# Performance work log

Measured on AMD Instinct MI355X. Metric: run time of the kernel, lower is better.

The kernel has to match this reference:

```python
import jax, jax.numpy as jnp
import numpy as np

D_MODEL = 1024
N_HEADS = 16
HEAD_DIM = D_MODEL // N_HEADS
LENGTHS = np.array([1536, 1024, 1400, 900, 1200, 1300, 1500, 1000])
OFFSETS = np.concatenate([[0], np.cumsum(LENGTHS)]).astype(np.int32)
N_TOT = int(OFFSETS[-1])
LN_EPS = 1e-5


def _pad_meta(offsets):
    # Static (numpy) gather indices: ragged concat [N,D] -> padded [B,Lmax,D]
    offsets = np.asarray(offsets)
    lengths = np.diff(offsets)
    lmax = int(lengths.max())
    tok = np.arange(lmax)[None, :]                      # [1, Lmax]
    valid = tok < lengths[:, None]                      # [B, Lmax] bool
    src = np.where(valid, offsets[:-1, None] + tok, 0)  # [B, Lmax] int
    return src, valid


def setup_inputs() -> dict:
    key = jax.random.key(0)
    ks = jax.random.split(key, 4)
    s = 1.0 / np.sqrt(D_MODEL)
    return {
        "x": jax.random.normal(ks[0], (N_TOT, D_MODEL), jnp.float32),
        "batch_offsets": jnp.asarray(OFFSETS, jnp.int32),
        "in_proj_w": jax.random.normal(ks[1], (3 * D_MODEL, D_MODEL), jnp.float32) * s,
        "in_proj_b": jnp.zeros((3 * D_MODEL,), jnp.float32),
        "out_w": jax.random.normal(ks[2], (D_MODEL, D_MODEL), jnp.float32) * s,
        "out_b": jnp.zeros((D_MODEL,), jnp.float32),
        "ln_g": jnp.ones((D_MODEL,), jnp.float32),
        "ln_b": jnp.zeros((D_MODEL,), jnp.float32),
    }


def reference(x, batch_offsets, in_proj_w, in_proj_b, out_w, out_b, ln_g, ln_b):
    src, valid = _pad_meta(np.asarray(batch_offsets))
    B, L = valid.shape
    vmask = jnp.asarray(valid)
    # deconcat_add_batch_dim: pad to [B, L, D]
    xp = x[src] * vmask[..., None]
    # pre-LayerNorm
    mu = jnp.mean(xp, axis=-1, keepdims=True)
    var = jnp.mean((xp - mu) ** 2, axis=-1, keepdims=True)
    h = (xp - mu) * jax.lax.rsqrt(var + LN_EPS) * ln_g + ln_b
    # fused qkv projection (torch MHA in_proj)
    qkv = h @ in_proj_w.T + in_proj_b                   # [B, L, 3D]
    q, k, v = jnp.split(qkv, 3, axis=-1)
    def heads(t):
        return t.reshape(B, L, N_HEADS, HEAD_DIM).transpose(0, 2, 1, 3)
    q, k, v = heads(q), heads(k), heads(v)              # [B, H, L, hd]
    scores = jnp.einsum("bhqd,bhkd->bhqk", q, k) / np.sqrt(HEAD_DIM)
    scores = jnp.where(vmask[:, None, None, :], scores, -jnp.inf)
    attn = jax.nn.softmax(scores, axis=-1)
    o = jnp.einsum("bhqk,bhkd->bhqd", attn, v)          # [B, H, L, hd]
    o = o.transpose(0, 2, 1, 3).reshape(B, L, D_MODEL)
    o = o @ out_w.T + out_b
    y = xp + o                                          # residual (dropout p=0)
    # remove_batch_dim_and_concat: unpad back to [N, D]
    return y[vmask]
```

## Files before the change

### kernel.cpp

```cpp
#include <hip/hip_runtime.h>
#include <hip/hip_bf16.h>
#include <stdint.h>

#define D_MODEL 1024
#define QKV_LD  3072
#define N_TOT   9860
#define M_PAD   9984
#define LN_EPS  1e-5f

typedef __bf16 bf16_t;
typedef __bf16 bf16x8 __attribute__((ext_vector_type(8)));
typedef float  f32x4  __attribute__((ext_vector_type(4)));
typedef float  f32x16 __attribute__((ext_vector_type(16)));
typedef uint32_t u32x4 __attribute__((ext_vector_type(4)));

__device__ inline unsigned short f2bf(float f) {
  __bf16 h = (__bf16)f;
  return __builtin_bit_cast(unsigned short, h);
}
__device__ inline int imin(int a, int b) { return a < b ? a : b; }

__device__ inline void plswap(uint32_t& a, uint32_t& b) {
  asm("v_permlane32_swap_b32 %0, %1" : "+v"(a), "+v"(b));
}

__device__ inline void gload_lds16(const bf16_t* g, void* l) {
  __builtin_amdgcn_global_load_lds(
      (const __attribute__((address_space(1))) unsigned int*)g,
      (__attribute__((address_space(3))) unsigned int*)l, 16, 0, 0);
}

__global__ __launch_bounds__(256) void cvt_weights(const float* __restrict__ w_in,
                                                   const float* __restrict__ w_out,
                                                   bf16_t* __restrict__ win,
                                                   bf16_t* __restrict__ wout) {
  const int n_in = QKV_LD * D_MODEL / 4;
  int i = blockIdx.x * 256 + threadIdx.x;
  const float* src;
  ushort4* dst;
  int j;
  if (i < n_in) { src = w_in; dst = (ushort4*)win; j = i; }
  else          { src = w_out; dst = (ushort4*)wout; j = i - n_in; }
  float4 v = ((const float4*)src)[j];
  dst[j] = make_ushort4(f2bf(v.x), f2bf(v.y), f2bf(v.z), f2bf(v.w));
}

__global__ __launch_bounds__(256) void ln_kernel(const float* __restrict__ x,
                                                 const float* __restrict__ g,
                                                 const float* __restrict__ b,
                                                 bf16_t* __restrict__ hout) {
  int row = blockIdx.x;
  int t = threadIdx.x;
  if (row >= N_TOT) {
    ((ushort4*)(hout + (size_t)row * D_MODEL))[t] = make_ushort4(0, 0, 0, 0);
    return;
  }
  float4 v = ((const float4*)(x + (size_t)row * D_MODEL))[t];
  float s  = v.x + v.y + v.z + v.w;
  float sq = v.x * v.x + v.y * v.y + v.z * v.z + v.w * v.w;
  #pragma unroll
  for (int off = 1; off < 64; off <<= 1) {
    s  += __shfl_xor(s, off);
    sq += __shfl_xor(sq, off);
  }
  __shared__ float ss[4], ssq[4];
  int wid = t >> 6;
  if ((t & 63) == 0) { ss[wid] = s; ssq[wid] = sq; }
  __syncthreads();
  s  = ss[0] + ss[1] + ss[2] + ss[3];
  sq = ssq[0] + ssq[1] + ssq[2] + ssq[3];
  float mu  = s * (1.0f / 1024.0f);
  float var = sq * (1.0f / 1024.0f) - mu * mu;
  float rs  = rsqrtf(var + LN_EPS);
  float4 gv = ((const float4*)g)[t];
  float4 bv = ((const float4*)b)[t];
  ushort4 o;
  o.x = f2bf((v.x - mu) * rs * gv.x + bv.x);
  o.y = f2bf((v.y - mu) * rs * gv.y + bv.y);
  o.z = f2bf((v.z - mu) * rs * gv.z + bv.z);
  o.w = f2bf((v.w - mu) * rs * gv.w + bv.w);
  ((ushort4*)(hout + (size_t)row * D_MODEL))[t] = o;
}

template<int NCOLS>
__global__ __launch_bounds__(512) void gemm256(const bf16_t* __restrict__ A,
                                               const bf16_t* __restrict__ B,
                                               const float* __restrict__ bias,
                                               bf16_t* __restrict__ Cbf) {
  constexpr int K = 1024, NKT = K / 64;
  constexpr int GX = M_PAD / 256;
  constexpr int NWG = GX * (NCOLS / 256);
  int bid = blockIdx.x;
  {
    constexpr int q = NWG / 8, r = NWG % 8;
    int x = bid & 7, o = bid >> 3;
    bid = (x < r ? x * (q + 1) : r * (q + 1) + (x - r) * q) + o;
  }
  const int tileM = bid % GX;
  const int tileN = bid / GX;
  const int t = threadIdx.x;
  const int lane = t & 63, wid = t >> 6;
  const int wr = wid >> 2, wc = wid & 3;

  __shared__ bf16_t As[2][256 * 64];
  __shared__ bf16_t Bs[2][256 * 64];

  f32x4 acc[8][4];
  #pragma unroll
  for (int m = 0; m < 8; ++m)
    #pragma unroll
    for (int n = 0; n < 4; ++n)
      acc[m][n] = f32x4{0.f, 0.f, 0.f, 0.f};

  const int rowA0 = tileM * 256, rowB0 = tileN * 256;
  const int lrow = lane >> 3;
  const int lch  = lane & 7;

  auto stage = [&](int buf, int kt) {
    const int k0 = kt * 64;
    #pragma unroll
    for (int i = 0; i < 4; ++i) {
      const int r  = wid * 32 + i * 8 + lrow;
      const int sc = lch ^ (r & 7);
      gload_lds16(A + (size_t)(rowA0 + r) * K + k0 + sc * 8,
                  (char*)&As[buf][(wid * 32 + i * 8) * 64]);
      gload_lds16(B + (size_t)(rowB0 + r) * K + k0 + sc * 8,
                  (char*)&Bs[buf][(wid * 32 + i * 8) * 64]);
    }
  };

  stage(0, 0);

  for (int kt = 0; kt < NKT; ++kt) {
    const int cur = kt & 1;
    if (kt + 1 < NKT) {
      stage(cur ^ 1, kt + 1);
      asm volatile("s_waitcnt vmcnt(8)" ::: "memory");
    } else {
      asm volatile("s_waitcnt vmcnt(0)" ::: "memory");
    }
    __builtin_amdgcn_s_barrier();
    __builtin_amdgcn_sched_barrier(0);

    const char* Ab = (const char*)&As[cur][0];
    const char* Bb = (const char*)&Bs[cur][0];

    bf16x8 bfr[4][2];
    #pragma unroll
    for (int n = 0; n < 4; ++n)
      #pragma unroll
      for (int ks = 0; ks < 2; ++ks) {
        int r = wc * 64 + n * 16 + (lane & 15);
        int c = ks * 4 + (lane >> 4);
        bfr[n][ks] = *(const bf16x8*)(Bb + r * 128 + ((c ^ (r & 7)) * 16));
      }
    #pragma unroll
    for (int p = 0; p < 4; ++p) {
      bf16x8 af[2][2];
      #pragma unroll
      for (int mm = 0; mm < 2; ++mm)
        #pragma unroll
        for (int ks = 0; ks < 2; ++ks) {
          int r = wr * 128 + (p * 2 + mm) * 16 + (lane & 15);
          int c = ks * 4 + (lane >> 4);
          af[mm][ks] = *(const bf16x8*)(Ab + r * 128 + ((c ^ (r & 7)) * 16));
        }
      __builtin_amdgcn_s_setprio(1);
      #pragma unroll
      for (int mm = 0; mm < 2; ++mm)
        #pragma unroll
        for (int n = 0; n < 4; ++n)
          #pragma unroll
          for (int ks = 0; ks < 2; ++ks)
            acc[p * 2 + mm][n] =
                __builtin_amdgcn_mfma_f32_16x16x32_bf16(af[mm][ks], bfr[n][ks],
                                                        acc[p * 2 + mm][n], 0, 0, 0);
      __builtin_amdgcn_s_setprio(0);
    }
    __builtin_amdgcn_sched_barrier(0);
    __builtin_amdgcn_s_barrier();
  }

  #pragma unroll
  for (int m = 0; m < 8; ++m) {
    int rb = tileM * 256 + wr * 128 + m * 16 + ((lane >> 4) << 2);
    #pragma unroll
    for (int n = 0; n < 4; ++n) {
      int cb = tileN * 256 + wc * 64 + n * 16 + (lane & 15);
      float bv = bias[cb];
      #pragma unroll
      for (int j = 0; j < 4; ++j)
        Cbf[(size_t)(rb + j) * NCOLS + cb] = (bf16_t)(acc[m][n][j] + bv);
    }
  }
}

template<int NCOLS, bool FINAL>
__global__ __launch_bounds__(256) void gemm_bt(const bf16_t* __restrict__ A,
                                               const bf16_t* __restrict__ B,
                                               const float* __restrict__ bias,
                                               bf16_t* __restrict__ Cbf,
                                               float* __restrict__ Cf,
                                               const float* __restrict__ resid) {
  constexpr int K = 1024;
  constexpr int GX = M_PAD / 128;
  constexpr int NWG = GX * (NCOLS / 128);
  int bid = blockIdx.x;
  bid = (bid & 7) * (NWG / 8) + (bid >> 3);
  const int tileM = bid % GX;
  const int tileN = bid / GX;
  const int t = threadIdx.x;
  const int lane = t & 63, wid = t >> 6;
  const int wr = wid >> 1, wc = wid & 1;

  __shared__ bf16_t Asm[128 * 64];
  __shared__ bf16_t Bsm[128 * 64];

  f32x4 acc[4][4];
  #pragma unroll
  for (int m = 0; m < 4; ++m)
    #pragma unroll
    for (int n = 0; n < 4; ++n)
      acc[m][n] = f32x4{0.f, 0.f, 0.f, 0.f};

  const int rowA0 = tileM * 128, rowB0 = tileN * 128;
  const int lrow = lane >> 3;
  const int lch  = lane & 7;

  for (int kt = 0; kt < K / 64; ++kt) {
    __syncthreads();
    const int k0 = kt * 64;
    #pragma unroll
    for (int i = 0; i < 4; ++i) {
      const int r  = wid * 32 + i * 8 + lrow;
      const int sc = lch ^ (r & 7);
      gload_lds16(A + (size_t)(rowA0 + r) * K + k0 + sc * 8,
                  (char*)Asm + (wid * 32 + i * 8) * 128);
      gload_lds16(B + (size_t)(rowB0 + r) * K + k0 + sc * 8,
                  (char*)Bsm + (wid * 32 + i * 8) * 128);
    }
    __syncthreads();
    #pragma unroll
    for (int ks = 0; ks < 2; ++ks) {
      bf16x8 af[4], bfr[4];
      #pragma unroll
      for (int m = 0; m < 4; ++m) {
        int r = wr * 64 + m * 16 + (lane & 15);
        int c = ks * 4 + (lane >> 4);
        af[m] = *(const bf16x8*)((const char*)Asm + r * 128 + ((c ^ (r & 7)) * 16));
      }
      #pragma unroll
      for (int n = 0; n < 4; ++n) {
        int r = wc * 64 + n * 16 + (lane & 15);
        int c = ks * 4 + (lane >> 4);
        bfr[n] = *(const bf16x8*)((const char*)Bsm + r * 128 + ((c ^ (r & 7)) * 16));
      }
      #pragma unroll
      for (int m = 0; m < 4; ++m)
        #pragma unroll
        for (int n = 0; n < 4; ++n)
          acc[m][n] = __builtin_amdgcn_mfma_f32_16x16x32_bf16(af[m], bfr[n], acc[m][n], 0, 0, 0);
    }
  }

  #pragma unroll
  for (int m = 0; m < 4; ++m) {
    int rb = tileM * 128 + wr * 64 + m * 16 + ((lane >> 4) << 2);
    #pragma unroll
    for (int n = 0; n < 4; ++n) {
      int cb = tileN * 128 + wc * 64 + n * 16 + (lane & 15);
      float bv = bias[cb];
      #pragma unroll
      for (int j = 0; j < 4; ++j) {
        int grow = rb + j;
        float val = acc[m][n][j] + bv;
        if constexpr (FINAL) {
          if (grow < N_TOT) {
            size_t idx = (size_t)grow * NCOLS + cb;
            Cf[idx] = resid[idx] + val;
          }
        } else {
          Cbf[(size_t)grow * NCOLS + cb] = (bf16_t)val;
        }
      }
    }
  }
}

__global__ __launch_bounds__(256) void transpose_v(const bf16_t* __restrict__ qkv,
                                                   bf16_t* __restrict__ vt) {
  __shared__ bf16_t tile[64][72];
  const int t = threadIdx.x;
  const int n0 = blockIdx.x * 64, c0 = blockIdx.y * 64;
  #pragma unroll
  for (int it = 0; it < 2; ++it) {
    int idx = it * 256 + t;
    int row = idx >> 3, ch = idx & 7;
    bf16x8 v = *(const bf16x8*)(qkv + (size_t)(n0 + row) * QKV_LD + 2048 + c0 + ch * 8);
    *(bf16x8*)(&tile[row][ch * 8]) = v;
  }
  __syncthreads();
  #pragma unroll
  for (int it = 0; it < 2; ++it) {
    int idx = it * 256 + t;
    int crow = idx >> 3, ng = idx & 7;
    bf16x8 o;
    #pragma unroll
    for (int i = 0; i < 8; ++i) o[i] = tile[ng * 8 + i][crow];
    *(bf16x8*)(vt + (size_t)(c0 + crow) * M_PAD + n0 + ng * 8) = o;
  }
}

__global__ __launch_bounds__(128) void attn_mfma(const bf16_t* __restrict__ qkv,
                                                 const bf16_t* __restrict__ vt,
                                                 bf16_t* __restrict__ obuf) {
  static const int off0_[8] = {0, 7360, 2560, 6060, 4860, 1536, 8860, 3960};
  static const int len_[8]  = {1536, 1500, 1400, 1300, 1200, 1024, 1000, 900};
  static const int ts_[9]   = {0, 24, 48, 70, 91, 110, 126, 142, 157};
  const int tt = blockIdx.x;
  const int h  = blockIdx.y;
  int b = 0;
  #pragma unroll
  for (int i = 1; i < 8; ++i) b += (tt >= ts_[i]);
  const int L     = len_[b];
  const int kbase = off0_[b];
  const int q0    = (tt - ts_[b]) * 64;
  const int tok0  = kbase + q0;
  const int nq    = imin(L - q0, 64);

  const int t = threadIdx.x;
  const int lane = t & 63, w = t >> 6;
  const int qcol = lane & 31, hi = lane >> 5;

  __shared__ char Ks[8192];
  __shared__ char Vs[8192];

  bf16x8 qf[4];
  {
    const bf16_t* qp = qkv + (size_t)(tok0 + w * 32 + qcol) * QKV_LD + h * 64;
    #pragma unroll
    for (int c = 0; c < 4; ++c) {
      bf16x8 v = *(const bf16x8*)(qp + c * 16 + hi * 8);
      #pragma unroll
      for (int i = 0; i < 8; ++i) v[i] = (__bf16)((float)v[i] * 0.125f);
      qf[c] = v;
    }
  }

  f32x16 accO[2];
  #pragma unroll
  for (int db = 0; db < 2; ++db)
    #pragma unroll
    for (int i = 0; i < 16; ++i) accO[db][i] = 0.f;
  float m_r  = -INFINITY;
  float lsum = 0.f;

  const int srow0 = t >> 3, sch = t & 7;

  int4 kreg[4];
  int2 vreg[4][2];
  auto load_tile = [&](int kv0) {
    #pragma unroll
    for (int it = 0; it < 4; ++it) {
      int row = srow0 + it * 16;
      kreg[it] = *(const int4*)(qkv + (size_t)(kbase + kv0 + row) * QKV_LD + 1024 + h * 64 + sch * 8);
      const bf16_t* vp = vt + (size_t)(h * 64 + row) * M_PAD + kbase + kv0 + sch * 8;
      vreg[it][0] = *(const int2*)vp;
      vreg[it][1] = *(const int2*)(vp + 4);
    }
  };

  load_tile(0);

  for (int kv0 = 0; kv0 < L; kv0 += 64) {
    const int nk = imin(L - kv0, 64);
    __syncthreads();
    #pragma unroll
    for (int it = 0; it < 4; ++it) {
      int row = srow0 + it * 16;
      int sw = ((sch ^ (row & 7)) * 16);
      *(int4*)(Ks + row * 128 + sw) = kreg[it];
      int4 vv;
      vv.x = vreg[it][0].x; vv.y = vreg[it][0].y;
      vv.z = vreg[it][1].x; vv.w = vreg[it][1].y;
      *(int4*)(Vs + row * 128 + sw) = vv;
    }
    __syncthreads();
    if (kv0 + 64 < L) load_tile(kv0 + 64);

    f32x16 accS[2];
    #pragma unroll
    for (int kb = 0; kb < 2; ++kb)
      #pragma unroll
      for (int i = 0; i < 16; ++i) accS[kb][i] = 0.f;
    __builtin_amdgcn_s_setprio(1);
    #pragma unroll
    for (int kb = 0; kb < 2; ++kb) {
      int key = kb * 32 + qcol;
      #pragma unroll
      for (int c = 0; c < 4; ++c) {
        bf16x8 kf = *(const bf16x8*)(Ks + key * 128 + (((2 * c + hi) ^ (key & 7)) * 16));
        accS[kb] = __builtin_amdgcn_mfma_f32_32x32x16_bf16(kf, qf[c], accS[kb], 0, 0, 0);
      }
    }
    __builtin_amdgcn_s_setprio(0);

    if (nk < 64) {
      #pragma unroll
      for (int kb = 0; kb < 2; ++kb)
        #pragma unroll
        for (int r = 0; r < 16; ++r)
          if (kb * 32 + (r & 3) + 8 * (r >> 2) + 4 * hi >= nk) accS[kb][r] = -INFINITY;
    }

    float mx = accS[0][0];
    #pragma unroll
    for (int r = 1; r < 16; ++r) mx = fmaxf(mx, accS[0][r]);
    #pragma unroll
    for (int r = 0; r < 16; ++r) mx = fmaxf(mx, accS[1][r]);
    mx = fmaxf(mx, __shfl_xor(mx, 32));

    if (!__all(mx <= m_r + 8.0f)) {
      float mnew = fmaxf(m_r, mx);
      float scl  = __expf(m_r - mnew);
      lsum *= scl;
      #pragma unroll
      for (int db = 0; db < 2; ++db)
        #pragma unroll
        for (int i = 0; i < 16; ++i) accO[db][i] *= scl;
      m_r = mnew;
    }

    bf16x8 pb[2][2];
    #pragma unroll
    for (int kb = 0; kb < 2; ++kb) {
      uint32_t G[4][2];
      #pragma unroll
      for (int j = 0; j < 4; ++j) {
        float p0 = __expf(accS[kb][4 * j + 0] - m_r);
        float p1 = __expf(accS[kb][4 * j + 1] - m_r);
        float p2 = __expf(accS[kb][4 * j + 2] - m_r);
        float p3 = __expf(accS[kb][4 * j + 3] - m_r);
        lsum += (p0 + p1) + (p2 + p3);
        G[j][0] = (uint32_t)f2bf(p0) | ((uint32_t)f2bf(p1) << 16);
        G[j][1] = (uint32_t)f2bf(p2) | ((uint32_t)f2bf(p3) << 16);
      }
      #pragma unroll
      for (int c = 0; c < 2; ++c) {
        uint32_t ax = G[2 * c][0], bx = G[2 * c + 1][0];
        uint32_t ay = G[2 * c][1], by = G[2 * c + 1][1];
        plswap(ax, bx);
        plswap(ay, by);
        u32x4 u; u[0] = ax; u[1] = ay; u[2] = bx; u[3] = by;
        pb[kb][c] = __builtin_bit_cast(bf16x8, u);
      }
    }

    __builtin_amdgcn_s_setprio(1);
    #pragma unroll
    for (int kb = 0; kb < 2; ++kb)
      #pragma unroll
      for (int c = 0; c < 2; ++c) {
        int ch = 4 * kb + 2 * c + hi;
        #pragma unroll
        for (int db = 0; db < 2; ++db) {
          int dim = db * 32 + qcol;
          bf16x8 vf = *(const bf16x8*)(Vs + dim * 128 + ((ch ^ (dim & 7)) * 16));
          accO[db] = __builtin_amdgcn_mfma_f32_32x32x16_bf16(vf, pb[kb][c], accO[db], 0, 0, 0);
        }
      }
    __builtin_amdgcn_s_setprio(0);
  }

  float l = lsum + __shfl_xor(lsum, 32);
  const int qlocal = w * 32 + qcol;
  if (qlocal < nq) {
    float inv = 1.f / l;
    bf16_t* op = obuf + (size_t)(tok0 + qlocal) * D_MODEL + h * 64;
    #pragma unroll
    for (int db = 0; db < 2; ++db)
      #pragma unroll
      for (int rr = 0; rr < 4; ++rr) {
        float v0 = accO[db][4 * rr + 0] * inv;
        float v1 = accO[db][4 * rr + 1] * inv;
        float v2 = accO[db][4 * rr + 2] * inv;
        float v3 = accO[db][4 * rr + 3] * inv;
        uint2 u;
        u.x = (uint32_t)f2bf(v0) | ((uint32_t)f2bf(v1) << 16);
        u.y = (uint32_t)f2bf(v2) | ((uint32_t)f2bf(v3) << 16);
        *(uint2*)(op + db * 32 + rr * 8 + hi * 4) = u;
      }
  }
}

extern "C" void kernel_launch(void* const* d_in, const int* in_sizes, int n_in,
                              void* d_out, int out_size, void* d_ws, size_t ws_size,
                              hipStream_t stream) {
  const float* x     = (const float*)d_in[0];
  const float* w_in  = (const float*)d_in[2];
  const float* b_in  = (const float*)d_in[3];
  const float* w_out = (const float*)d_in[4];
  const float* b_out = (const float*)d_in[5];
  const float* ln_g  = (const float*)d_in[6];
  const float* ln_b  = (const float*)d_in[7];
  float* out = (float*)d_out;

  char* ws = (char*)d_ws;
  const size_t SZ_H   = (size_t)M_PAD * D_MODEL * 2;
  const size_t SZ_QKV = (size_t)M_PAD * QKV_LD * 2;
  const size_t SZ_O   = SZ_H;
  const size_t SZ_WIN = (size_t)QKV_LD * D_MODEL * 2;
  const size_t SZ_WO  = (size_t)D_MODEL * D_MODEL * 2;
  if (ws_size < SZ_H + SZ_QKV + SZ_O + SZ_WIN + SZ_WO) return;

  bf16_t* h_bf    = (bf16_t*)ws;
  bf16_t* qkv_bf  = (bf16_t*)(ws + SZ_H);
  bf16_t* o_bf    = (bf16_t*)(ws + SZ_H + SZ_QKV);
  bf16_t* win_bf  = (bf16_t*)(ws + SZ_H + SZ_QKV + SZ_O);
  bf16_t* wout_bf = (bf16_t*)(ws + SZ_H + SZ_QKV + SZ_O + SZ_WIN);

  cvt_weights<<<(QKV_LD * D_MODEL / 4 + D_MODEL * D_MODEL / 4) / 256, 256, 0, stream>>>(
      w_in, w_out, win_bf, wout_bf);

  ln_kernel<<<M_PAD, 256, 0, stream>>>(x, ln_g, ln_b, h_bf);

  gemm256<QKV_LD><<<(M_PAD / 256) * (QKV_LD / 256), 512, 0, stream>>>(
      h_bf, win_bf, b_in, qkv_bf);

  bf16_t* vt = h_bf;
  transpose_v<<<dim3(M_PAD / 64, D_MODEL / 64), 256, 0, stream>>>(qkv_bf, vt);

  attn_mfma<<<dim3(157, 16), 128, 0, stream>>>(qkv_bf, vt, o_bf);

  gemm_bt<D_MODEL, true><<<(M_PAD / 128) * (D_MODEL / 128), 256, 0, stream>>>(
      o_bf, wout_bf, b_out, nullptr, out, x);
}
```

Baseline: 340.5 us.

## Double-buffer K/V via direct global-to-LDS loads, 128-query attention tiles

```diff
diff --git a/kernel.cpp b/kernel.cpp
--- a/kernel.cpp
+++ b/kernel.cpp
@@ -289,6 +289,8 @@
 
 __global__ __launch_bounds__(256) void transpose_v(const bf16_t* __restrict__ qkv,
                                                    bf16_t* __restrict__ vt) {
+  static const int OFF_[8] = {0, 1536, 2560, 3960, 4860, 6060, 7360, 8860};
+  static const int SH_[8]  = {0, 0, 0, 0, 4, 4, 8, 12};
   __shared__ bf16_t tile[64][72];
   const int t = threadIdx.x;
   const int n0 = blockIdx.x * 64, c0 = blockIdx.y * 64;
@@ -304,19 +306,46 @@
   for (int it = 0; it < 2; ++it) {
     int idx = it * 256 + t;
     int crow = idx >> 3, ng = idx & 7;
+    int tok0 = n0 + ng * 8;
+    if (tok0 >= N_TOT) continue;
     bf16x8 o;
     #pragma unroll
     for (int i = 0; i < 8; ++i) o[i] = tile[ng * 8 + i][crow];
-    *(bf16x8*)(vt + (size_t)(c0 + crow) * M_PAD + n0 + ng * 8) = o;
-  }
-}
-
-__global__ __launch_bounds__(128) void attn_mfma(const bf16_t* __restrict__ qkv,
+    int b0 = 0;
+    #pragma unroll
+    for (int i = 1; i < 8; ++i) b0 += (tok0 >= OFF_[i]);
+    bool fast = (tok0 + 7 < N_TOT);
+    if (fast) {
+      int b7 = 0;
+      #pragma unroll
+      for (int i = 1; i < 8; ++i) b7 += (tok0 + 7 >= OFF_[i]);
+      fast = (b7 == b0);
+    }
+    bf16_t* vrow = vt + (size_t)(c0 + crow) * M_PAD;
+    if (fast) {
+      *(bf16x8*)(vrow + tok0 + SH_[b0]) = o;
+    } else {
+      #pragma unroll
+      for (int i = 0; i < 8; ++i) {
+        int tok = tok0 + i;
+        if (tok < N_TOT) {
+          int bb = 0;
+          #pragma unroll
+          for (int k = 1; k < 8; ++k) bb += (tok >= OFF_[k]);
+          vrow[tok + SH_[bb]] = o[i];
+        }
+      }
+    }
+  }
+}
+
+__global__ __launch_bounds__(256) void attn_mfma(const bf16_t* __restrict__ qkv,
                                                  const bf16_t* __restrict__ vt,
                                                  bf16_t* __restrict__ obuf) {
   static const int off0_[8] = {0, 7360, 2560, 6060, 4860, 1536, 8860, 3960};
+  static const int vcol_[8] = {0, 7368, 2560, 6064, 4864, 1536, 8872, 3960};
   static const int len_[8]  = {1536, 1500, 1400, 1300, 1200, 1024, 1000, 900};
-  static const int ts_[9]   = {0, 24, 48, 70, 91, 110, 126, 142, 157};
+  static const int ts_[9]   = {0, 12, 24, 35, 46, 56, 64, 72, 80};
   const int tt = blockIdx.x;
   const int h  = blockIdx.y;
   int b = 0;
@@ -324,17 +353,19 @@
   for (int i = 1; i < 8; ++i) b += (tt >= ts_[i]);
   const int L     = len_[b];
   const int kbase = off0_[b];
-  const int q0    = (tt - ts_[b]) * 64;
+  const int vcol  = vcol_[b];
+  const int q0    = (tt - ts_[b]) * 128;
   const int tok0  = kbase + q0;
-  const int nq    = imin(L - q0, 64);
+  const int nq    = imin(L - q0, 128);
 
   const int t = threadIdx.x;
   const int lane = t & 63, w = t >> 6;
   const int qcol = lane & 31, hi = lane >> 5;
 
-  __shared__ char Ks[8192];
-  __shared__ char Vs[8192];
-
+  __shared__ char Ks[2][8192];
+  __shared__ char Vs[2][8192];
+
+  const float qs = 0.125f * 1.44269504f;
   bf16x8 qf[4];
   {
     const bf16_t* qp = qkv + (size_t)(tok0 + w * 32 + qcol) * QKV_LD + h * 64;
@@ -342,7 +373,7 @@
     for (int c = 0; c < 4; ++c) {
       bf16x8 v = *(const bf16x8*)(qp + c * 16 + hi * 8);
       #pragma unroll
-      for (int i = 0; i < 8; ++i) v[i] = (__bf16)((float)v[i] * 0.125f);
+      for (int i = 0; i < 8; ++i) v[i] = (__bf16)((float)v[i] * qs);
       qf[c] = v;
     }
   }
@@ -355,38 +386,32 @@
   float m_r  = -INFINITY;
   float lsum = 0.f;
 
-  const int srow0 = t >> 3, sch = t & 7;
-
-  int4 kreg[4];
-  int2 vreg[4][2];
-  auto load_tile = [&](int kv0) {
-    #pragma unroll
-    for (int it = 0; it < 4; ++it) {
-      int row = srow0 + it * 16;
-      kreg[it] = *(const int4*)(qkv + (size_t)(kbase + kv0 + row) * QKV_LD + 1024 + h * 64 + sch * 8);
-      const bf16_t* vp = vt + (size_t)(h * 64 + row) * M_PAD + kbase + kv0 + sch * 8;
-      vreg[it][0] = *(const int2*)vp;
-      vreg[it][1] = *(const int2*)(vp + 4);
+  const int srow = w * 8 + (lane >> 3);
+  const int sch  = lane & 7;
+  const int sc   = sch ^ (srow & 7);
+
+  auto stage = [&](int buf, int kv0) {
+    #pragma unroll
+    for (int it = 0; it < 2; ++it) {
+      int row = srow + it * 32;
+      gload_lds16(qkv + (size_t)(kbase + kv0 + row) * QKV_LD + 1024 + h * 64 + sc * 8,
+                  &Ks[buf][w * 1024 + it * 4096]);
+      gload_lds16(vt + (size_t)(h * 64 + row) * M_PAD + vcol + kv0 + sc * 8,
+                  &Vs[buf][w * 1024 + it * 4096]);
     }
   };
 
-  load_tile(0);
-
-  for (int kv0 = 0; kv0 < L; kv0 += 64) {
-    const int nk = imin(L - kv0, 64);
+  stage(0, 0);
+  int cur = 0;
+  const int nt = (L + 63) >> 6;
+
+  for (int ti = 0; ti < nt; ++ti) {
+    const int nk = imin(L - ti * 64, 64);
     __syncthreads();
-    #pragma unroll
-    for (int it = 0; it < 4; ++it) {
-      int row = srow0 + it * 16;
-      int sw = ((sch ^ (row & 7)) * 16);
-      *(int4*)(Ks + row * 128 + sw) = kreg[it];
-      int4 vv;
-      vv.x = vreg[it][0].x; vv.y = vreg[it][0].y;
-      vv.z = vreg[it][1].x; vv.w = vreg[it][1].y;
-      *(int4*)(Vs + row * 128 + sw) = vv;
-    }
-    __syncthreads();
-    if (kv0 + 64 < L) load_tile(kv0 + 64);
+    if (ti + 1 < nt) stage(cur ^ 1, (ti + 1) * 64);
+
+    const char* Kb = Ks[cur];
+    const char* Vb = Vs[cur];
 
     f32x16 accS[2];
     #pragma unroll
@@ -399,7 +424,7 @@
       int key = kb * 32 + qcol;
       #pragma unroll
       for (int c = 0; c < 4; ++c) {
-        bf16x8 kf = *(const bf16x8*)(Ks + key * 128 + (((2 * c + hi) ^ (key & 7)) * 16));
+        bf16x8 kf = *(const bf16x8*)(Kb + key * 128 + (((2 * c + hi) ^ (key & 7)) * 16));
         accS[kb] = __builtin_amdgcn_mfma_f32_32x32x16_bf16(kf, qf[c], accS[kb], 0, 0, 0);
       }
     }
@@ -420,9 +445,9 @@
     for (int r = 0; r < 16; ++r) mx = fmaxf(mx, accS[1][r]);
     mx = fmaxf(mx, __shfl_xor(mx, 32));
 
-    if (!__all(mx <= m_r + 8.0f)) {
+    if (!__all(mx <= m_r + 11.54f)) {
       float mnew = fmaxf(m_r, mx);
-      float scl  = __expf(m_r - mnew);
+      float scl  = exp2f(m_r - mnew);
       lsum *= scl;
       #pragma unroll
       for (int db = 0; db < 2; ++db)
@@ -437,10 +462,10 @@
       uint32_t G[4][2];
       #pragma unroll
       for (int j = 0; j < 4; ++j) {
-        float p0 = __expf(accS[kb][4 * j + 0] - m_r);
-        float p1 = __expf(accS[kb][4 * j + 1] - m_r);
-        float p2 = __expf(accS[kb][4 * j + 2] - m_r);
-        float p3 = __expf(accS[kb][4 * j + 3] - m_r);
+        float p0 = exp2f(accS[kb][4 * j + 0] - m_r);
+        float p1 = exp2f(accS[kb][4 * j + 1] - m_r);
+        float p2 = exp2f(accS[kb][4 * j + 2] - m_r);
+        float p3 = exp2f(accS[kb][4 * j + 3] - m_r);
         lsum += (p0 + p1) + (p2 + p3);
         G[j][0] = (uint32_t)f2bf(p0) | ((uint32_t)f2bf(p1) << 16);
         G[j][1] = (uint32_t)f2bf(p2) | ((uint32_t)f2bf(p3) << 16);
@@ -465,11 +490,12 @@
         #pragma unroll
         for (int db = 0; db < 2; ++db) {
           int dim = db * 32 + qcol;
-          bf16x8 vf = *(const bf16x8*)(Vs + dim * 128 + ((ch ^ (dim & 7)) * 16));
+          bf16x8 vf = *(const bf16x8*)(Vb + dim * 128 + ((ch ^ (dim & 7)) * 16));
           accO[db] = __builtin_amdgcn_mfma_f32_32x32x16_bf16(vf, pb[kb][c], accO[db], 0, 0, 0);
         }
       }
     __builtin_amdgcn_s_setprio(0);
+    cur ^= 1;
   }
 
   float l = lsum + __shfl_xor(lsum, 32);
@@ -530,7 +556,7 @@
   bf16_t* vt = h_bf;
   transpose_v<<<dim3(M_PAD / 64, D_MODEL / 64), 256, 0, stream>>>(qkv_bf, vt);
 
-  attn_mfma<<<dim3(157, 16), 128, 0, stream>>>(qkv_bf, vt, o_bf);
+  attn_mfma<<<dim3(80, 16), 256, 0, stream>>>(qkv_bf, vt, o_bf);
 
   gemm_bt<D_MODEL, true><<<(M_PAD / 128) * (D_MODEL / 128), 256, 0, stream>>>(
       o_bf, wout_bf, b_out, nullptr, out, x);
```

After: 324.7 us. 4.6% less time.
